# Performance work log

Hardware: AMD Instinct MI355X
Metric: run time of the kernel (lower is better)

Reference implementation:

```python
import jax, jax.numpy as jnp
import numpy as np

N_NODES = 100000


def gcn_conv(x, src, dst, W, b):
    # x: [N, F_in]; src/dst include self-loops; symmetric degree normalization (PyG GCNConv)
    n = x.shape[0]
    xw = x @ W  # [N, F_out]
    ones = jnp.ones(dst.shape[0], dtype=xw.dtype)
    deg = jax.ops.segment_sum(ones, dst, num_segments=n)  # in-degree incl. self-loop
    dinv = jnp.where(deg > 0, jax.lax.rsqrt(deg), 0.0)
    norm = dinv[src] * dinv[dst]  # [E]
    msg = xw[src] * norm[:, None]  # gather + per-edge scale
    out = jax.ops.segment_sum(msg, dst, num_segments=n)  # scatter-add aggregation
    return out + b


def setup_inputs() -> dict:
    key = jax.random.key(0)
    ks = jax.random.split(key, 6)
    F_in = 512
    E = 3200000
    x = jax.random.normal(ks[0], (N_NODES, F_in), dtype=jnp.float32)
    edge_index = jax.random.randint(ks[1], (2, E), 0, N_NODES, dtype=jnp.int64)
    W1 = jax.random.normal(ks[2], (F_in, 16), dtype=jnp.float32) * (1.0 / np.sqrt(F_in))
    b1 = jnp.zeros((16,), dtype=jnp.float32)
    W2 = jax.random.normal(ks[3], (16, 16), dtype=jnp.float32) * 0.25
    b2 = jnp.zeros((16,), dtype=jnp.float32)
    fc_w = jax.random.normal(ks[4], (16, 1), dtype=jnp.float32) * 0.25
    fc_b = jnp.zeros((1,), dtype=jnp.float32)
    return {"x": x, "edge_index": edge_index, "W1": W1, "b1": b1,
            "W2": W2, "b2": b2, "fc_w": fc_w, "fc_b": fc_b}


def reference(x, edge_index, W1, b1, W2, b2, fc_w, fc_b):
    n = x.shape[0]
    loop = jnp.arange(n, dtype=edge_index.dtype)
    src = jnp.concatenate([edge_index[0], loop])  # add self-loops
    dst = jnp.concatenate([edge_index[1], loop])
    h = jax.nn.relu(gcn_conv(x, src, dst, W1, b1))
    h = jax.nn.relu(gcn_conv(h, src, dst, W2, b2))
    g = jnp.mean(h, axis=0, keepdims=True)  # global_mean_pool, single graph -> [1, 16]
    return g @ fc_w + fc_b  # [1, 1]
```

## Files before the change

### kernel.cpp

```cpp
#include <hip/hip_runtime.h>
#include <stdint.h>

#define F_IN 512
#define F_OUT 16
#define CB_SHIFT 8
#define CB_W 256
#define PER 6250
#define SORT_CAP 6400

__device__ inline float4 f4_shfl_xor(float4 v, int mask) {
    float4 r;
    r.x = __shfl_xor(v.x, mask);
    r.y = __shfl_xor(v.y, mask);
    r.z = __shfl_xor(v.z, mask);
    r.w = __shfl_xor(v.w, mask);
    return r;
}

__global__ __launch_bounds__(256) void k_chist(const int* __restrict__ ei, int E, int K1, int B,
                                               int* __restrict__ cntT) {
    __shared__ int h[512];
    int t = threadIdx.x;
    for (int i = t; i < K1; i += 256) h[i] = 0;
    __syncthreads();
    int e0 = blockIdx.x * PER, e1 = min(E, e0 + PER);
    for (int e = e0 + t; e < e1; e += 256)
        atomicAdd(&h[ei[(size_t)E + e] >> CB_SHIFT], 1);
    __syncthreads();
    for (int i = t; i < K1; i += 256) cntT[(size_t)i * B + blockIdx.x] = h[i];
}

__global__ __launch_bounds__(512) void k_btot(const int* __restrict__ cntT, int B, int K1,
                                              int* __restrict__ bucketBase, int* __restrict__ bucketCnt) {
    __shared__ int sm[512];
    int k = threadIdx.x;
    int tot = 0;
    if (k < K1) {
        const int4* row = (const int4*)(cntT + (size_t)k * B);
        for (int b = 0; b < B / 4; b++) {
            int4 v = row[b];
            tot += v.x + v.y + v.z + v.w;
        }
    }
    sm[k] = tot;
    __syncthreads();
    for (int off = 1; off < 512; off <<= 1) {
        int add = (k >= off) ? sm[k - off] : 0;
        __syncthreads();
        sm[k] += add;
        __syncthreads();
    }
    if (k < K1) { bucketBase[k] = sm[k] - tot; bucketCnt[k] = tot; }
}

__global__ __launch_bounds__(512) void k_bbase(const int* __restrict__ cntT, int B,
                                               const int* __restrict__ bucketBase,
                                               int* __restrict__ baseT) {
    __shared__ int sm[512];
    int k = blockIdx.x, t = threadIdx.x;
    int v = (t < B) ? cntT[(size_t)k * B + t] : 0;
    sm[t] = v;
    __syncthreads();
    for (int off = 1; off < 512; off <<= 1) {
        int add = (t >= off) ? sm[t - off] : 0;
        __syncthreads();
        sm[t] += add;
        __syncthreads();
    }
    if (t < B) baseT[(size_t)k * B + t] = bucketBase[k] + sm[t] - v;
}

__global__ __launch_bounds__(512) void k_csort(const int* __restrict__ ei, int E, int K1, int B,
                                               const int* __restrict__ baseT, unsigned* __restrict__ part) {
    __shared__ unsigned sorted[SORT_CAP];
    __shared__ int h[512], lb[512], cur[512], gb[512];
    int t = threadIdx.x;
    int e0 = blockIdx.x * PER, e1 = min(E, e0 + PER);
    h[t] = 0;
    __syncthreads();
    for (int e = e0 + t; e < e1; e += 512)
        atomicAdd(&h[ei[(size_t)E + e] >> CB_SHIFT], 1);
    __syncthreads();
    int v = h[t];
    lb[t] = v;
    __syncthreads();
    for (int off = 1; off < 512; off <<= 1) {
        int add = (t >= off) ? lb[t - off] : 0;
        __syncthreads();
        lb[t] += add;
        __syncthreads();
    }
    int excl = lb[t] - v;
    __syncthreads();
    lb[t] = excl;
    cur[t] = excl;
    if (t < K1) gb[t] = baseT[(size_t)t * B + blockIdx.x];
    __syncthreads();
    for (int e = e0 + t; e < e1; e += 512) {
        int s = ei[e];
        int d = ei[(size_t)E + e];
        int pos = atomicAdd(&cur[d >> CB_SHIFT], 1);
        sorted[pos] = ((unsigned)s << CB_SHIFT) | (unsigned)(d & (CB_W - 1));
    }
    __syncthreads();
    int g16 = t >> 4, ln = t & 15;
    for (int k = g16; k < K1; k += 32) {
        int s0 = lb[k];
        int s1 = cur[k];
        int g  = gb[k];
        for (int i = s0 + ln; i < s1; i += 16)
            part[(size_t)g + (i - s0)] = sorted[i];
    }
}

__global__ __launch_bounds__(512) void k_prep2(const unsigned* __restrict__ part,
                                               const int* __restrict__ bucketBase, const int* __restrict__ bucketCnt,
                                               int* __restrict__ hist, float* __restrict__ dinv,
                                               int* __restrict__ offsets, int* __restrict__ csr, int N) {
    __shared__ int fh[CB_W], fb[CB_W], cur[CB_W];
    int k = blockIdx.x, t = threadIdx.x;
    int base = bucketBase[k], cnt = bucketCnt[k];
    int d0 = k << CB_SHIFT;
    if (t < CB_W) fh[t] = 0;
    __syncthreads();
    for (int i = t; i < cnt; i += 512)
        atomicAdd(&fh[part[(size_t)base + i] & (CB_W - 1)], 1);
    __syncthreads();
    int v = 0;
    if (t < CB_W) { v = fh[t]; fb[t] = v; }
    __syncthreads();
    for (int off = 1; off < CB_W; off <<= 1) {
        int add = (t >= off && t < CB_W) ? fb[t - off] : 0;
        __syncthreads();
        if (t < CB_W) fb[t] += add;
        __syncthreads();
    }
    if (t < CB_W) {
        int excl = fb[t] - v;
        int n = d0 + t;
        if (n < N) {
            offsets[n] = base + excl;
            hist[n] = v;
            dinv[n] = rsqrtf((float)(v + 1));
        }
        cur[t] = excl;
    }
    __syncthreads();
    for (int i = t; i < cnt; i += 512) {
        unsigned e = part[(size_t)base + i];
        int pos = atomicAdd(&cur[e & (CB_W - 1)], 1);
        csr[(size_t)base + pos] = (int)(e >> CB_SHIFT);
    }
}

__global__ __launch_bounds__(256) void k_gemm1(const float* __restrict__ x, const float* __restrict__ W1,
                                               const float* __restrict__ dinv, float* __restrict__ xw1p, int N) {
    int n = blockIdx.x * 256 + threadIdx.x;
    if (n >= N) return;
    const float4* xr = (const float4*)(x + (size_t)n * F_IN);
    const float4* wr = (const float4*)W1;

    float acc[16];
#pragma unroll
    for (int j = 0; j < 16; j++) acc[j] = 0.f;

#pragma unroll 4
    for (int kk = 0; kk < 128; kk++) {
        float4 xv = xr[kk];
#pragma unroll
        for (int i = 0; i < 4; i++) {
            float xs = (i == 0) ? xv.x : (i == 1) ? xv.y : (i == 2) ? xv.z : xv.w;
#pragma unroll
            for (int q = 0; q < 4; q++) {
                float4 wv = wr[kk * 16 + i * 4 + q];
                acc[q*4+0] = fmaf(xs, wv.x, acc[q*4+0]);
                acc[q*4+1] = fmaf(xs, wv.y, acc[q*4+1]);
                acc[q*4+2] = fmaf(xs, wv.z, acc[q*4+2]);
                acc[q*4+3] = fmaf(xs, wv.w, acc[q*4+3]);
            }
        }
    }
    float dn = dinv[n];
    float4* orow = (float4*)(xw1p + (size_t)n * F_OUT);
#pragma unroll
    for (int q = 0; q < 4; q++)
        orow[q] = make_float4(dn*acc[q*4+0], dn*acc[q*4+1], dn*acc[q*4+2], dn*acc[q*4+3]);
}

__global__ __launch_bounds__(256) void k_agg1(const float* __restrict__ xw, const int* __restrict__ offsets,
                                              const int* __restrict__ hist, const float* __restrict__ dinv,
                                              const int* __restrict__ csr, const float* __restrict__ b1,
                                              const float* __restrict__ W2, float* __restrict__ xw2p, int N) {
    __shared__ float W2s[256];
    if (threadIdx.x < 256) W2s[threadIdx.x] = W2[threadIdx.x];
    __syncthreads();

    int lane = threadIdx.x & 63;
    int wave = threadIdx.x >> 6;
    int grp  = lane >> 4;
    int sub  = lane & 15;
    int eo   = sub >> 2;
    int q    = sub & 3;
    int node = blockIdx.x * 16 + wave * 4 + grp;
    if (node >= N) return;

    int start = offsets[node], cnt = hist[node];
    float dn = dinv[node];
    float4 a0 = make_float4(0.f,0.f,0.f,0.f), a1 = a0, a2 = a0, a3 = a0;
    int i = 0;
    for (; i + 32 <= cnt; i += 32) {
        int s0 = csr[start + i + eo];
        int s1 = csr[start + i + 4 + eo];
        int s2 = csr[start + i + 8 + eo];
        int s3 = csr[start + i + 12 + eo];
        int s4 = csr[start + i + 16 + eo];
        int s5 = csr[start + i + 20 + eo];
        int s6 = csr[start + i + 24 + eo];
        int s7 = csr[start + i + 28 + eo];
        float4 v0 = ((const float4*)(xw + (size_t)s0 * F_OUT))[q];
        float4 v1 = ((const float4*)(xw + (size_t)s1 * F_OUT))[q];
        float4 v2 = ((const float4*)(xw + (size_t)s2 * F_OUT))[q];
        float4 v3 = ((const float4*)(xw + (size_t)s3 * F_OUT))[q];
        float4 v4 = ((const float4*)(xw + (size_t)s4 * F_OUT))[q];
        float4 v5 = ((const float4*)(xw + (size_t)s5 * F_OUT))[q];
        float4 v6 = ((const float4*)(xw + (size_t)s6 * F_OUT))[q];
        float4 v7 = ((const float4*)(xw + (size_t)s7 * F_OUT))[q];
        a0.x+=v0.x; a0.y+=v0.y; a0.z+=v0.z; a0.w+=v0.w;
        a1.x+=v1.x; a1.y+=v1.y; a1.z+=v1.z; a1.w+=v1.w;
        a2.x+=v2.x; a2.y+=v2.y; a2.z+=v2.z; a2.w+=v2.w;
        a3.x+=v3.x; a3.y+=v3.y; a3.z+=v3.z; a3.w+=v3.w;
        a0.x+=v4.x; a0.y+=v4.y; a0.z+=v4.z; a0.w+=v4.w;
        a1.x+=v5.x; a1.y+=v5.y; a1.z+=v5.z; a1.w+=v5.w;
        a2.x+=v6.x; a2.y+=v6.y; a2.z+=v6.z; a2.w+=v6.w;
        a3.x+=v7.x; a3.y+=v7.y; a3.z+=v7.z; a3.w+=v7.w;
    }
    for (; i + 16 <= cnt; i += 16) {
        int s0 = csr[start + i + eo];
        int s1 = csr[start + i + 4 + eo];
        int s2 = csr[start + i + 8 + eo];
        int s3 = csr[start + i + 12 + eo];
        float4 v0 = ((const float4*)(xw + (size_t)s0 * F_OUT))[q];
        float4 v1 = ((const float4*)(xw + (size_t)s1 * F_OUT))[q];
        float4 v2 = ((const float4*)(xw + (size_t)s2 * F_OUT))[q];
        float4 v3 = ((const float4*)(xw + (size_t)s3 * F_OUT))[q];
        a0.x+=v0.x; a0.y+=v0.y; a0.z+=v0.z; a0.w+=v0.w;
        a1.x+=v1.x; a1.y+=v1.y; a1.z+=v1.z; a1.w+=v1.w;
        a2.x+=v2.x; a2.y+=v2.y; a2.z+=v2.z; a2.w+=v2.w;
        a3.x+=v3.x; a3.y+=v3.y; a3.z+=v3.z; a3.w+=v3.w;
    }
    for (; i + 8 <= cnt; i += 8) {
        int s0 = csr[start + i + eo];
        int s1 = csr[start + i + 4 + eo];
        float4 v0 = ((const float4*)(xw + (size_t)s0 * F_OUT))[q];
        float4 v1 = ((const float4*)(xw + (size_t)s1 * F_OUT))[q];
        a0.x+=v0.x; a0.y+=v0.y; a0.z+=v0.z; a0.w+=v0.w;
        a1.x+=v1.x; a1.y+=v1.y; a1.z+=v1.z; a1.w+=v1.w;
    }
    for (; i < cnt; i += 4) {
        if (i + eo < cnt) {
            int s0 = csr[start + i + eo];
            float4 v0 = ((const float4*)(xw + (size_t)s0 * F_OUT))[q];
            a0.x+=v0.x; a0.y+=v0.y; a0.z+=v0.z; a0.w+=v0.w;
        }
    }
    float4 acc;
    acc.x = a0.x+a1.x+a2.x+a3.x;
    acc.y = a0.y+a1.y+a2.y+a3.y;
    acc.z = a0.z+a1.z+a2.z+a3.z;
    acc.w = a0.w+a1.w+a2.w+a3.w;
    { float4 u = f4_shfl_xor(acc, 4); acc.x+=u.x; acc.y+=u.y; acc.z+=u.z; acc.w+=u.w; }
    { float4 u = f4_shfl_xor(acc, 8); acc.x+=u.x; acc.y+=u.y; acc.z+=u.z; acc.w+=u.w; }

    float4 sv = ((const float4*)(xw + (size_t)node * F_OUT))[q];
    float4 bq = ((const float4*)b1)[q];
    float4 h;
    h.x = fmaxf(dn * (acc.x + sv.x) + bq.x, 0.f);
    h.y = fmaxf(dn * (acc.y + sv.y) + bq.y, 0.f);
    h.z = fmaxf(dn * (acc.z + sv.z) + bq.z, 0.f);
    h.w = fmaxf(dn * (acc.w + sv.w) + bq.w, 0.f);

    float o = 0.f;
#pragma unroll
    for (int a = 0; a < 4; a++) {
        int src = (grp << 4) + a;
        float h0 = __shfl(h.x, src);
        float h1 = __shfl(h.y, src);
        float h2 = __shfl(h.z, src);
        float h3 = __shfl(h.w, src);
        o += h0 * W2s[(a*4+0)*16 + sub] + h1 * W2s[(a*4+1)*16 + sub]
           + h2 * W2s[(a*4+2)*16 + sub] + h3 * W2s[(a*4+3)*16 + sub];
    }
    xw2p[(size_t)node * F_OUT + sub] = dn * o;
}

__global__ __launch_bounds__(256) void k_agg2(const float* __restrict__ xw, const int* __restrict__ offsets,
                                              const int* __restrict__ hist, const float* __restrict__ dinv,
                                              const int* __restrict__ csr, const float* __restrict__ b2,
                                              float* __restrict__ partials, int N) {
    int lane = threadIdx.x & 63;
    int wave = threadIdx.x >> 6;
    int grp  = lane >> 4;
    int sub  = lane & 15;
    int eo   = sub >> 2;
    int q    = sub & 3;
    int node = blockIdx.x * 16 + wave * 4 + grp;

    float4 m = make_float4(0.f, 0.f, 0.f, 0.f);
    if (node < N) {
        int start = offsets[node], cnt = hist[node];
        float dn = dinv[node];
        float4 a0 = make_float4(0.f,0.f,0.f,0.f), a1 = a0, a2 = a0, a3 = a0;
        int i = 0;
        for (; i + 32 <= cnt; i += 32) {
            int s0 = csr[start + i + eo];
            int s1 = csr[start + i + 4 + eo];
            int s2 = csr[start + i + 8 + eo];
            int s3 = csr[start + i + 12 + eo];
            int s4 = csr[start + i + 16 + eo];
            int s5 = csr[start + i + 20 + eo];
            int s6 = csr[start + i + 24 + eo];
            int s7 = csr[start + i + 28 + eo];
            float4 v0 = ((const float4*)(xw + (size_t)s0 * F_OUT))[q];
            float4 v1 = ((const float4*)(xw + (size_t)s1 * F_OUT))[q];
            float4 v2 = ((const float4*)(xw + (size_t)s2 * F_OUT))[q];
            float4 v3 = ((const float4*)(xw + (size_t)s3 * F_OUT))[q];
            float4 v4 = ((const float4*)(xw + (size_t)s4 * F_OUT))[q];
            float4 v5 = ((const float4*)(xw + (size_t)s5 * F_OUT))[q];
            float4 v6 = ((const float4*)(xw + (size_t)s6 * F_OUT))[q];
            float4 v7 = ((const float4*)(xw + (size_t)s7 * F_OUT))[q];
            a0.x+=v0.x; a0.y+=v0.y; a0.z+=v0.z; a0.w+=v0.w;
            a1.x+=v1.x; a1.y+=v1.y; a1.z+=v1.z; a1.w+=v1.w;
            a2.x+=v2.x; a2.y+=v2.y; a2.z+=v2.z; a2.w+=v2.w;
            a3.x+=v3.x; a3.y+=v3.y; a3.z+=v3.z; a3.w+=v3.w;
            a0.x+=v4.x; a0.y+=v4.y; a0.z+=v4.z; a0.w+=v4.w;
            a1.x+=v5.x; a1.y+=v5.y; a1.z+=v5.z; a1.w+=v5.w;
            a2.x+=v6.x; a2.y+=v6.y; a2.z+=v6.z; a2.w+=v6.w;
            a3.x+=v7.x; a3.y+=v7.y; a3.z+=v7.z; a3.w+=v7.w;
        }
        for (; i + 16 <= cnt; i += 16) {
            int s0 = csr[start + i + eo];
            int s1 = csr[start + i + 4 + eo];
            int s2 = csr[start + i + 8 + eo];
            int s3 = csr[start + i + 12 + eo];
            float4 v0 = ((const float4*)(xw + (size_t)s0 * F_OUT))[q];
            float4 v1 = ((const float4*)(xw + (size_t)s1 * F_OUT))[q];
            float4 v2 = ((const float4*)(xw + (size_t)s2 * F_OUT))[q];
            float4 v3 = ((const float4*)(xw + (size_t)s3 * F_OUT))[q];
            a0.x+=v0.x; a0.y+=v0.y; a0.z+=v0.z; a0.w+=v0.w;
            a1.x+=v1.x; a1.y+=v1.y; a1.z+=v1.z; a1.w+=v1.w;
            a2.x+=v2.x; a2.y+=v2.y; a2.z+=v2.z; a2.w+=v2.w;
            a3.x+=v3.x; a3.y+=v3.y; a3.z+=v3.z; a3.w+=v3.w;
        }
        for (; i + 8 <= cnt; i += 8) {
            int s0 = csr[start + i + eo];
            int s1 = csr[start + i + 4 + eo];
            float4 v0 = ((const float4*)(xw + (size_t)s0 * F_OUT))[q];
            float4 v1 = ((const float4*)(xw + (size_t)s1 * F_OUT))[q];
            a0.x+=v0.x; a0.y+=v0.y; a0.z+=v0.z; a0.w+=v0.w;
            a1.x+=v1.x; a1.y+=v1.y; a1.z+=v1.z; a1.w+=v1.w;
        }
        for (; i < cnt; i += 4) {
            if (i + eo < cnt) {
                int s0 = csr[start + i + eo];
                float4 v0 = ((const float4*)(xw + (size_t)s0 * F_OUT))[q];
                a0.x+=v0.x; a0.y+=v0.y; a0.z+=v0.z; a0.w+=v0.w;
            }
        }
        float4 acc;
        acc.x = a0.x+a1.x+a2.x+a3.x;
        acc.y = a0.y+a1.y+a2.y+a3.y;
        acc.z = a0.z+a1.z+a2.z+a3.z;
        acc.w = a0.w+a1.w+a2.w+a3.w;
        { float4 u = f4_shfl_xor(acc, 4); acc.x+=u.x; acc.y+=u.y; acc.z+=u.z; acc.w+=u.w; }
        { float4 u = f4_shfl_xor(acc, 8); acc.x+=u.x; acc.y+=u.y; acc.z+=u.z; acc.w+=u.w; }
        float4 sv = ((const float4*)(xw + (size_t)node * F_OUT))[q];
        float4 bq = ((const float4*)b2)[q];
        if (eo == 0) {
            m.x = fmaxf(dn * (acc.x + sv.x) + bq.x, 0.f);
            m.y = fmaxf(dn * (acc.y + sv.y) + bq.y, 0.f);
            m.z = fmaxf(dn * (acc.z + sv.z) + bq.z, 0.f);
            m.w = fmaxf(dn * (acc.w + sv.w) + bq.w, 0.f);
        }
    }
    { float4 u = f4_shfl_xor(m, 16); m.x+=u.x; m.y+=u.y; m.z+=u.z; m.w+=u.w; }
    { float4 u = f4_shfl_xor(m, 32); m.x+=u.x; m.y+=u.y; m.z+=u.z; m.w+=u.w; }
    __shared__ float smf[4][16];
    if (lane < 4) {
        smf[wave][q*4+0] = m.x;
        smf[wave][q*4+1] = m.y;
        smf[wave][q*4+2] = m.z;
        smf[wave][q*4+3] = m.w;
    }
    __syncthreads();
    if (threadIdx.x < 16) {
        float s = smf[0][threadIdx.x] + smf[1][threadIdx.x] + smf[2][threadIdx.x] + smf[3][threadIdx.x];
        partials[(size_t)blockIdx.x * 16 + threadIdx.x] = s;
    }
}

__global__ void k_final(const float* __restrict__ partials, int NB, const float* __restrict__ fc_w,
                        const float* __restrict__ fc_b, float* __restrict__ out, float invN) {
    __shared__ float sm[64][16];
    int t = threadIdx.x;
    int g = t >> 4, j = t & 15;
    float s = 0.0f;
    for (int bk = g; bk < NB; bk += 64) s += partials[(size_t)bk * 16 + j];
    sm[g][j] = s;
    __syncthreads();
    for (int str = 32; str > 0; str >>= 1) {
        if (g < str) sm[g][j] += sm[g + str][j];
        __syncthreads();
    }
    if (t == 0) {
        float acc = fc_b[0];
#pragma unroll
        for (int jj = 0; jj < 16; jj++) acc += sm[0][jj] * invN * fc_w[jj];
        out[0] = acc;
    }
}

extern "C" void kernel_launch(void* const* d_in, const int* in_sizes, int n_in,
                              void* d_out, int out_size, void* d_ws, size_t ws_size,
                              hipStream_t stream) {
    const float* x   = (const float*)d_in[0];
    const int*   ei  = (const int*)d_in[1];
    const float* W1  = (const float*)d_in[2];
    const float* b1  = (const float*)d_in[3];
    const float* W2  = (const float*)d_in[4];
    const float* b2  = (const float*)d_in[5];
    const float* fcw = (const float*)d_in[6];
    const float* fcb = (const float*)d_in[7];
    float* out = (float*)d_out;

    int N = in_sizes[0] / F_IN;
    int E = in_sizes[1] / 2;
    int K1 = (N + CB_W - 1) >> CB_SHIFT;
    int B1 = (E + PER - 1) / PER;

    char* p = (char*)d_ws;
    auto alloc = [&](size_t bytes) {
        void* r = (void*)p;
        p += (bytes + 255) & ~(size_t)255;
        return r;
    };
    int*   cntT       = (int*)alloc((size_t)K1 * B1 * 4);
    int*   baseT      = (int*)alloc((size_t)K1 * B1 * 4);
    int*   bucketBase = (int*)alloc((size_t)K1 * 4);
    int*   bucketCnt  = (int*)alloc((size_t)K1 * 4);
    int*   hist       = (int*)alloc((size_t)N * 4);
    int*   offsets    = (int*)alloc((size_t)N * 4);
    float* dinv       = (float*)alloc((size_t)N * 4);
    int*   csr        = (int*)alloc((size_t)E * 4);
    unsigned* part    = (unsigned*)alloc((size_t)E * 4);
    int NB_NODE = (N + 15) / 16;
    float* partials = (float*)alloc((size_t)NB_NODE * 16 * 4);
    float* xw1p = (float*)part;
    float* xw2p = xw1p + (size_t)N * F_OUT;

    k_chist<<<B1, 256, 0, stream>>>(ei, E, K1, B1, cntT);
    k_btot<<<1, 512, 0, stream>>>(cntT, B1, K1, bucketBase, bucketCnt);
    k_bbase<<<K1, 512, 0, stream>>>(cntT, B1, bucketBase, baseT);
    k_csort<<<B1, 512, 0, stream>>>(ei, E, K1, B1, baseT, part);
    k_prep2<<<K1, 512, 0, stream>>>(part, bucketBase, bucketCnt, hist, dinv, offsets, csr, N);

    k_gemm1<<<(N + 255) / 256, 256, 0, stream>>>(x, W1, dinv, xw1p, N);
    k_agg1<<<NB_NODE, 256, 0, stream>>>(xw1p, offsets, hist, dinv, csr, b1, W2, xw2p, N);
    k_agg2<<<NB_NODE, 256, 0, stream>>>(xw2p, offsets, hist, dinv, csr, b2, partials, N);
    k_final<<<1, 1024, 0, stream>>>(partials, NB_NODE, fcw, fcb, out, 1.0f / (float)N);
}
```

Baseline: 237.0 us.

## Overlap first-layer GEMM with CSR-build kernels via block-range fusion

Splits the x@W1 GEMM into two halves and runs each half in extra blocks appended to the histogram kernel and the counting-sort kernel. The memory-bound GEMM then runs concurrently with the integer sort passes instead of after them. Because dinv is not yet known during the GEMM, a separate scaling kernel applies the degree normalization afterwards. xw1/xw2 get their own buffers rather than aliasing the partition buffer. The cost is an extra kernel launch and an extra read/write pass over xw1. The histogram kernel also moves from 256 to 512 threads.

```diff
diff --git a/kernel.cpp b/kernel.cpp
--- a/kernel.cpp
+++ b/kernel.cpp
@@ -17,17 +17,56 @@
     return r;
 }
 
-__global__ __launch_bounds__(256) void k_chist(const int* __restrict__ ei, int E, int K1, int B,
-                                               int* __restrict__ cntT) {
-    __shared__ int h[512];
-    int t = threadIdx.x;
-    for (int i = t; i < K1; i += 256) h[i] = 0;
-    __syncthreads();
-    int e0 = blockIdx.x * PER, e1 = min(E, e0 + PER);
-    for (int e = e0 + t; e < e1; e += 256)
-        atomicAdd(&h[ei[(size_t)E + e] >> CB_SHIFT], 1);
-    __syncthreads();
-    for (int i = t; i < K1; i += 256) cntT[(size_t)i * B + blockIdx.x] = h[i];
+__device__ inline void gemm1_body(const float* __restrict__ x, const float* __restrict__ W1,
+                                  float* __restrict__ xw1, int N, int n) {
+    if (n >= N) return;
+    const float4* xr = (const float4*)(x + (size_t)n * F_IN);
+    const float4* wr = (const float4*)W1;
+
+    float acc[16];
+#pragma unroll
+    for (int j = 0; j < 16; j++) acc[j] = 0.f;
+
+#pragma unroll 4
+    for (int kk = 0; kk < 128; kk++) {
+        float4 xv = xr[kk];
+#pragma unroll
+        for (int i = 0; i < 4; i++) {
+            float xs = (i == 0) ? xv.x : (i == 1) ? xv.y : (i == 2) ? xv.z : xv.w;
+#pragma unroll
+            for (int q = 0; q < 4; q++) {
+                float4 wv = wr[kk * 16 + i * 4 + q];
+                acc[q*4+0] = fmaf(xs, wv.x, acc[q*4+0]);
+                acc[q*4+1] = fmaf(xs, wv.y, acc[q*4+1]);
+                acc[q*4+2] = fmaf(xs, wv.z, acc[q*4+2]);
+                acc[q*4+3] = fmaf(xs, wv.w, acc[q*4+3]);
+            }
+        }
+    }
+    float4* orow = (float4*)(xw1 + (size_t)n * F_OUT);
+#pragma unroll
+    for (int q = 0; q < 4; q++)
+        orow[q] = make_float4(acc[q*4+0], acc[q*4+1], acc[q*4+2], acc[q*4+3]);
+}
+
+__global__ __launch_bounds__(512) void k_fuseA(const int* __restrict__ ei, int E, int K1, int B,
+                                               int* __restrict__ cntT,
+                                               const float* __restrict__ x, const float* __restrict__ W1,
+                                               float* __restrict__ xw1, int N, int nodeOff) {
+    if ((int)blockIdx.x < B) {
+        __shared__ int h[512];
+        int t = threadIdx.x;
+        for (int i = t; i < K1; i += 512) h[i] = 0;
+        __syncthreads();
+        int e0 = blockIdx.x * PER, e1 = min(E, e0 + PER);
+        for (int e = e0 + t; e < e1; e += 512)
+            atomicAdd(&h[ei[(size_t)E + e] >> CB_SHIFT], 1);
+        __syncthreads();
+        for (int i = t; i < K1; i += 512) cntT[(size_t)i * B + blockIdx.x] = h[i];
+    } else {
+        int n = ((int)blockIdx.x - B) * 512 + (int)threadIdx.x + nodeOff;
+        gemm1_body(x, W1, xw1, N, n);
+    }
 }
 
 __global__ __launch_bounds__(512) void k_btot(const int* __restrict__ cntT, int B, int K1,
@@ -70,46 +109,53 @@
     if (t < B) baseT[(size_t)k * B + t] = bucketBase[k] + sm[t] - v;
 }
 
-__global__ __launch_bounds__(512) void k_csort(const int* __restrict__ ei, int E, int K1, int B,
-                                               const int* __restrict__ baseT, unsigned* __restrict__ part) {
-    __shared__ unsigned sorted[SORT_CAP];
-    __shared__ int h[512], lb[512], cur[512], gb[512];
-    int t = threadIdx.x;
-    int e0 = blockIdx.x * PER, e1 = min(E, e0 + PER);
-    h[t] = 0;
-    __syncthreads();
-    for (int e = e0 + t; e < e1; e += 512)
-        atomicAdd(&h[ei[(size_t)E + e] >> CB_SHIFT], 1);
-    __syncthreads();
-    int v = h[t];
-    lb[t] = v;
-    __syncthreads();
-    for (int off = 1; off < 512; off <<= 1) {
-        int add = (t >= off) ? lb[t - off] : 0;
-        __syncthreads();
-        lb[t] += add;
-        __syncthreads();
-    }
-    int excl = lb[t] - v;
-    __syncthreads();
-    lb[t] = excl;
-    cur[t] = excl;
-    if (t < K1) gb[t] = baseT[(size_t)t * B + blockIdx.x];
-    __syncthreads();
-    for (int e = e0 + t; e < e1; e += 512) {
-        int s = ei[e];
-        int d = ei[(size_t)E + e];
-        int pos = atomicAdd(&cur[d >> CB_SHIFT], 1);
-        sorted[pos] = ((unsigned)s << CB_SHIFT) | (unsigned)(d & (CB_W - 1));
-    }
-    __syncthreads();
-    int g16 = t >> 4, ln = t & 15;
-    for (int k = g16; k < K1; k += 32) {
-        int s0 = lb[k];
-        int s1 = cur[k];
-        int g  = gb[k];
-        for (int i = s0 + ln; i < s1; i += 16)
-            part[(size_t)g + (i - s0)] = sorted[i];
+__global__ __launch_bounds__(512) void k_fuseD(const int* __restrict__ ei, int E, int K1, int B,
+                                               const int* __restrict__ baseT, unsigned* __restrict__ part,
+                                               const float* __restrict__ x, const float* __restrict__ W1,
+                                               float* __restrict__ xw1, int N, int nodeOff) {
+    if ((int)blockIdx.x < B) {
+        __shared__ unsigned sorted[SORT_CAP];
+        __shared__ int h[512], lb[512], cur[512], gb[512];
+        int t = threadIdx.x;
+        int e0 = blockIdx.x * PER, e1 = min(E, e0 + PER);
+        h[t] = 0;
+        __syncthreads();
+        for (int e = e0 + t; e < e1; e += 512)
+            atomicAdd(&h[ei[(size_t)E + e] >> CB_SHIFT], 1);
+        __syncthreads();
+        int v = h[t];
+        lb[t] = v;
+        __syncthreads();
+        for (int off = 1; off < 512; off <<= 1) {
+            int add = (t >= off) ? lb[t - off] : 0;
+            __syncthreads();
+            lb[t] += add;
+            __syncthreads();
+        }
+        int excl = lb[t] - v;
+        __syncthreads();
+        lb[t] = excl;
+        cur[t] = excl;
+        if (t < K1) gb[t] = baseT[(size_t)t * B + blockIdx.x];
+        __syncthreads();
+        for (int e = e0 + t; e < e1; e += 512) {
+            int s = ei[e];
+            int d = ei[(size_t)E + e];
+            int pos = atomicAdd(&cur[d >> CB_SHIFT], 1);
+            sorted[pos] = ((unsigned)s << CB_SHIFT) | (unsigned)(d & (CB_W - 1));
+        }
+        __syncthreads();
+        int g16 = t >> 4, ln = t & 15;
+        for (int k = g16; k < K1; k += 32) {
+            int s0 = lb[k];
+            int s1 = cur[k];
+            int g  = gb[k];
+            for (int i = s0 + ln; i < s1; i += 16)
+                part[(size_t)g + (i - s0)] = sorted[i];
+        }
+    } else {
+        int n = ((int)blockIdx.x - B) * 512 + (int)threadIdx.x + nodeOff;
+        gemm1_body(x, W1, xw1, N, n);
     }
 }
 
@@ -153,38 +199,15 @@
     }
 }
 
-__global__ __launch_bounds__(256) void k_gemm1(const float* __restrict__ x, const float* __restrict__ W1,
-                                               const float* __restrict__ dinv, float* __restrict__ xw1p, int N) {
-    int n = blockIdx.x * 256 + threadIdx.x;
-    if (n >= N) return;
-    const float4* xr = (const float4*)(x + (size_t)n * F_IN);
-    const float4* wr = (const float4*)W1;
-
-    float acc[16];
-#pragma unroll
-    for (int j = 0; j < 16; j++) acc[j] = 0.f;
-
-#pragma unroll 4
-    for (int kk = 0; kk < 128; kk++) {
-        float4 xv = xr[kk];
-#pragma unroll
-        for (int i = 0; i < 4; i++) {
-            float xs = (i == 0) ? xv.x : (i == 1) ? xv.y : (i == 2) ? xv.z : xv.w;
-#pragma unroll
-            for (int q = 0; q < 4; q++) {
-                float4 wv = wr[kk * 16 + i * 4 + q];
-                acc[q*4+0] = fmaf(xs, wv.x, acc[q*4+0]);
-                acc[q*4+1] = fmaf(xs, wv.y, acc[q*4+1]);
-                acc[q*4+2] = fmaf(xs, wv.z, acc[q*4+2]);
-                acc[q*4+3] = fmaf(xs, wv.w, acc[q*4+3]);
-            }
-        }
-    }
-    float dn = dinv[n];
-    float4* orow = (float4*)(xw1p + (size_t)n * F_OUT);
-#pragma unroll
-    for (int q = 0; q < 4; q++)
-        orow[q] = make_float4(dn*acc[q*4+0], dn*acc[q*4+1], dn*acc[q*4+2], dn*acc[q*4+3]);
+__global__ __launch_bounds__(512) void k_scale(float* __restrict__ xw1, const float* __restrict__ dinv, int N) {
+    int i = blockIdx.x * 512 + threadIdx.x;
+    if (i < N * 4) {
+        int node = i >> 2;
+        float dn = dinv[node];
+        float4* p = (float4*)xw1 + i;
+        float4 v = *p;
+        *p = make_float4(v.x * dn, v.y * dn, v.z * dn, v.w * dn);
+    }
 }
 
 __global__ __launch_bounds__(256) void k_agg1(const float* __restrict__ xw, const int* __restrict__ offsets,
@@ -452,18 +475,23 @@
     float* dinv       = (float*)alloc((size_t)N * 4);
     int*   csr        = (int*)alloc((size_t)E * 4);
     unsigned* part    = (unsigned*)alloc((size_t)E * 4);
+    float* xw1p       = (float*)alloc((size_t)N * F_OUT * 4);
+    float* xw2p       = (float*)alloc((size_t)N * F_OUT * 4);
     int NB_NODE = (N + 15) / 16;
     float* partials = (float*)alloc((size_t)NB_NODE * 16 * 4);
-    float* xw1p = (float*)part;
-    float* xw2p = xw1p + (size_t)N * F_OUT;
-
-    k_chist<<<B1, 256, 0, stream>>>(ei, E, K1, B1, cntT);
+
+    int GT = (N + 511) / 512;
+    int GA = GT / 2;
+    int GB = GT - GA;
+    int offA = 0, offB = GA * 512;
+
+    k_fuseA<<<B1 + GA, 512, 0, stream>>>(ei, E, K1, B1, cntT, x, W1, xw1p, N, offA);
     k_btot<<<1, 512, 0, stream>>>(cntT, B1, K1, bucketBase, bucketCnt);
     k_bbase<<<K1, 512, 0, stream>>>(cntT, B1, bucketBase, baseT);
-    k_csort<<<B1, 512, 0, stream>>>(ei, E, K1, B1, baseT, part);
+    k_fuseD<<<B1 + GB, 512, 0, stream>>>(ei, E, K1, B1, baseT, part, x, W1, xw1p, N, offB);
     k_prep2<<<K1, 512, 0, stream>>>(part, bucketBase, bucketCnt, hist, dinv, offsets, csr, N);
-
-    k_gemm1<<<(N + 255) / 256, 256, 0, stream>>>(x, W1, dinv, xw1p, N);
+    k_scale<<<(N * 4 + 511) / 512, 512, 0, stream>>>(xw1p, dinv, N);
+
     k_agg1<<<NB_NODE, 256, 0, stream>>>(xw1p, offsets, hist, dinv, csr, b1, W2, xw2p, N);
     k_agg2<<<NB_NODE, 256, 0, stream>>>(xw2p, offsets, hist, dinv, csr, b2, partials, N);
     k_final<<<1, 1024, 0, stream>>>(partials, NB_NODE, fcw, fcb, out, 1.0f / (float)N);
```

After: 265.0 us. +11.8%, slower.
